# Kernel tuning notes

Measured on AMD Instinct MI355X. Metric: run time of the kernel, lower is better.

## Reference

```python
import jax, jax.numpy as jnp
import numpy as np

B, S, D, H = 2, 2048, 1024, 16
DK = D // H  # 64


def rotate_half(x):
    d = x.shape[-1]
    x1, x2 = x[..., : d // 2], x[..., d // 2 :]
    return jnp.concatenate([-x2, x1], axis=-1)


def apply_rope(q, k):
    # q, k: [B, H, S, DK]
    d_k = q.shape[-1]
    seq_len = q.shape[-2]
    theta = 10000.0 ** (-2.0 / d_k * jnp.arange(d_k // 2, dtype=q.dtype))
    positions = jnp.arange(seq_len, dtype=q.dtype)
    angles = jnp.outer(positions, theta)                    # [S, DK/2]
    cos = jnp.tile(jnp.cos(angles), (1, 2))                 # [S, DK]
    sin = jnp.tile(jnp.sin(angles), (1, 2))
    q = q * cos + rotate_half(q) * sin
    k = k * cos + rotate_half(k) * sin
    return q, k


def setup_inputs() -> dict:
    key = jax.random.key(0)
    ks = jax.random.split(key, 9)
    std = 1.0 / np.sqrt(D)
    x = jax.random.normal(ks[0], (B, S, D), dtype=jnp.float32)
    # mask True = masked (code uses masked_fill(mask, -inf)); causal mask
    mask = jnp.triu(jnp.ones((S, S), dtype=bool), k=1)[None, None, :, :]
    mask = jnp.broadcast_to(mask, (B, 1, S, S))
    Wq = jax.random.uniform(ks[1], (D, D), jnp.float32, -std, std)
    bq = jax.random.uniform(ks[2], (D,), jnp.float32, -std, std)
    Wk = jax.random.uniform(ks[3], (D, D), jnp.float32, -std, std)
    bk = jax.random.uniform(ks[4], (D,), jnp.float32, -std, std)
    Wv = jax.random.uniform(ks[5], (D, D), jnp.float32, -std, std)
    bv = jax.random.uniform(ks[6], (D,), jnp.float32, -std, std)
    Wo = jax.random.uniform(ks[7], (D, D), jnp.float32, -std, std)
    bo = jax.random.uniform(ks[8], (D,), jnp.float32, -std, std)
    return {"x": x, "mask": mask, "Wq": Wq, "bq": bq, "Wk": Wk, "bk": bk,
            "Wv": Wv, "bv": bv, "Wo": Wo, "bo": bo}


def reference(x, mask, Wq, bq, Wk, bk, Wv, bv, Wo, bo):
    b, s, d = x.shape
    # projections -> [B, H, S, DK]
    q = (x @ Wq + bq).reshape(b, s, H, DK).transpose(0, 2, 1, 3)
    k = (x @ Wk + bk).reshape(b, s, H, DK).transpose(0, 2, 1, 3)
    v = (x @ Wv + bv).reshape(b, s, H, DK).transpose(0, 2, 1, 3)
    q, k = apply_rope(q, k)
    scores = jnp.einsum("bhqd,bhkd->bhqk", q, k) / np.sqrt(DK)
    scores = jnp.where(mask, -jnp.inf, scores)
    probs = jax.nn.softmax(scores, axis=-1)
    attn = jnp.einsum("bhqk,bhkd->bhqd", probs, v)
    o = attn.transpose(0, 2, 1, 3).reshape(b, s, H * DK)
    return o @ Wo + bo
```

## Files before the change

### kernel.cpp

```cpp
#include <hip/hip_runtime.h>
#include <hip/hip_bf16.h>
#include <math.h>

typedef __hip_bfloat16 bf16;
typedef __attribute__((ext_vector_type(8))) short short8;
typedef __attribute__((ext_vector_type(4))) short s16x4;
typedef __attribute__((ext_vector_type(4))) float f32x4;

#define B_  2
#define S_  2048
#define D_  1024
#define H_  16
#define DK_ 64

#define QSCALE 0.18033688011112043f
#define EXPOFF 11.541560327111707f

__device__ inline short bfs(float f) { return __builtin_bit_cast(short, __float2bfloat16(f)); }

#define GLL16(gptr, lptr)                                                        \
    __builtin_amdgcn_global_load_lds(                                            \
        (const __attribute__((address_space(1))) void*)(gptr),                   \
        (__attribute__((address_space(3))) void*)(lptr), 16, 0, 0)

#if __has_builtin(__builtin_amdgcn_mfma_f32_16x16x16bf16_1k)
#define MFMA_16x16x16(A, Bv, C) __builtin_amdgcn_mfma_f32_16x16x16bf16_1k(A, Bv, C, 0, 0, 0)
#elif __has_builtin(__builtin_amdgcn_mfma_f32_16x16x16_bf16)
#define MFMA_16x16x16(A, Bv, C) __builtin_amdgcn_mfma_f32_16x16x16_bf16(A, Bv, C, 0, 0, 0)
#else
static __device__ inline f32x4 mfma16_asm(s16x4 a, s16x4 b, f32x4 c) {
    f32x4 d;
    asm volatile("v_mfma_f32_16x16x16_bf16 %0, %1, %2, %3\n\ts_nop 7\n\ts_nop 7"
                 : "=v"(d) : "v"(a), "v"(b), "v"(c));
    return d;
}
#define MFMA_16x16x16(A, Bv, C) mfma16_asm(A, Bv, C)
#endif

__global__ __launch_bounds__(256)
void prep_k(const float* __restrict__ x,
            const float* __restrict__ W0, const float* __restrict__ W1,
            const float* __restrict__ W2, const float* __restrict__ W3,
            bf16* __restrict__ cx, bf16* __restrict__ Wt)
{
    const int z = blockIdx.z;
    const int t = threadIdx.x;
    if (z == 4) {
        const int bid = blockIdx.y * 16 + blockIdx.x;
        #pragma unroll
        for (int i = 0; i < 16; i++) {
            const size_t g = ((size_t)bid * 256 + t) * 4 + (size_t)i * 262144;
            const float4 v = *(const float4*)(x + g);
            s16x4 o = { bfs(v.x), bfs(v.y), bfs(v.z), bfs(v.w) };
            *(s16x4*)(cx + g) = o;
        }
        return;
    }
    __shared__ float Lt[64][65];
    const float* W = (z == 0) ? W0 : (z == 1) ? W1 : (z == 2) ? W2 : W3;
    bf16* dst = Wt + (size_t)z * D_ * D_;
    const int k0 = blockIdx.y * 64, n0 = blockIdx.x * 64;
    #pragma unroll
    for (int p = 0; p < 4; p++) {
        const int idx = p * 256 + t;
        const int row = idx >> 4, cb = (idx & 15) * 4;
        const float4 v = *(const float4*)(W + (size_t)(k0 + row) * D_ + n0 + cb);
        Lt[cb + 0][row] = v.x; Lt[cb + 1][row] = v.y;
        Lt[cb + 2][row] = v.z; Lt[cb + 3][row] = v.w;
    }
    __syncthreads();
    #pragma unroll
    for (int p = 0; p < 4; p++) {
        const int idx = p * 256 + t;
        const int n = idx >> 4, kb = (idx & 15) * 4;
        s16x4 o = { bfs(Lt[n][kb]), bfs(Lt[n][kb + 1]), bfs(Lt[n][kb + 2]), bfs(Lt[n][kb + 3]) };
        *(s16x4*)(dst + (size_t)(n0 + n) * D_ + k0 + kb) = o;
    }
}

template<int MODE, int TM>
__global__ __launch_bounds__(256)
void gemm_k(const bf16* __restrict__ A, const bf16* __restrict__ WtAll,
            const float* __restrict__ b0, const float* __restrict__ b1,
            const float* __restrict__ b2,
            bf16* __restrict__ d0, bf16* __restrict__ d1, bf16* __restrict__ d2,
            float* __restrict__ fout)
{
    constexpr int K = D_;
    constexpr int MT = (B_ * S_) / TM;
    constexpr int AI = TM / 64;
    const int L = (int)blockIdx.x;
    const int m0 = (L & (MT - 1)) * TM;
    const int rest = L / MT;
    const int z = (MODE == 0) ? (rest >> 4) : 3;
    const int n0 = (MODE == 0) ? (rest & 15) * 64 : rest * 64;
    const bf16* W = WtAll + (size_t)z * D_ * D_;
    const float* bias = (MODE == 1) ? b0 : ((z == 0) ? b0 : (z == 1) ? b1 : b2);

    __shared__ __align__(16) short As[TM * 32];
    __shared__ __align__(16) short Bs[64 * 32];

    const int t = threadIdx.x;
    const int wave = t >> 6, lane = t & 63, quad = lane >> 4, l16 = lane & 15;
    const int wm = wave * (TM / 4);

    const bf16* gA0 = A + (size_t)(m0 + (t >> 2)) * K + (t & 3) * 8;
    const bf16* gA1 = gA0 + (size_t)64 * K;
    const bf16* gW0 = W + (size_t)(n0 + (t >> 2)) * K + (t & 3) * 8;
    const int wb = wave * 512;

    f32x4 acc[AI][4] = {};

    for (int k0 = 0; k0 < K; k0 += 32) {
        __syncthreads();
        GLL16(gA0 + k0, &As[wb]);
        if (TM == 128) GLL16(gA1 + k0, &As[2048 + wb]);
        GLL16(gW0 + k0, &Bs[wb]);
        __syncthreads();
        short8 af[AI], bfv[4];
        #pragma unroll
        for (int i = 0; i < AI; i++) af[i] = *(const short8*)&As[(wm + i * 16 + l16) * 32 + quad * 8];
        #pragma unroll
        for (int j = 0; j < 4; j++) bfv[j] = *(const short8*)&Bs[(j * 16 + l16) * 32 + quad * 8];
        #pragma unroll
        for (int i = 0; i < AI; i++)
            #pragma unroll
            for (int j = 0; j < 4; j++)
                acc[i][j] = __builtin_amdgcn_mfma_f32_16x16x32_bf16(af[i], bfv[j], acc[i][j], 0, 0, 0);
    }

    if (MODE == 1) {
        #pragma unroll
        for (int j = 0; j < 4; j++) {
            const int ncol = n0 + j * 16 + l16;
            const float bb = bias[ncol];
            #pragma unroll
            for (int i = 0; i < AI; i++) {
                const int mbase = m0 + wm + i * 16 + quad * 4;
                #pragma unroll
                for (int r = 0; r < 4; r++)
                    fout[(size_t)(mbase + r) * D_ + ncol] = acc[i][j][r] + bb;
            }
        }
    } else if (z == 2) {
        const int h = n0 >> 6;
        #pragma unroll
        for (int j = 0; j < 4; j++) {
            const int ncol = n0 + j * 16 + l16;
            const float bb = bias[ncol];
            const int dk = ncol & 63;
            #pragma unroll
            for (int i = 0; i < AI; i++) {
                const int mbase = m0 + wm + i * 16 + quad * 4;
                #pragma unroll
                for (int r = 0; r < 4; r++) {
                    const int m = mbase + r;
                    const int b = m >> 11, s = m & (S_ - 1);
                    d2[(((size_t)(b * H_ + h)) * DK_ + dk) * S_ + s] = __float2bfloat16(acc[i][j][r] + bb);
                }
            }
        }
    } else {
        bf16* dst = z ? d1 : d0;
        const float sc = z ? 1.0f : QSCALE;
        const int h = n0 >> 6;
        #pragma unroll
        for (int j = 0; j < 2; j++) {
            const int dk = j * 16 + l16;
            const float th = exp2f((float)dk * -0.41524101186092029f);
            const float blo = bias[(h << 6) + dk];
            const float bhi = bias[(h << 6) + dk + 32];
            #pragma unroll
            for (int i = 0; i < AI; i++) {
                #pragma unroll
                for (int r = 0; r < 4; r++) {
                    const int m = m0 + wm + i * 16 + quad * 4 + r;
                    const int b = m >> 11, s = m & (S_ - 1);
                    float sn, cs;
                    sincosf((float)s * th, &sn, &cs);
                    const float v1 = acc[i][j][r] + blo;
                    const float v2 = acc[i][j + 2][r] + bhi;
                    bf16* p = dst + (((size_t)(b * H_ + h)) * S_ + s) * DK_;
                    p[dk]      = __float2bfloat16((v1 * cs - v2 * sn) * sc);
                    p[dk + 32] = __float2bfloat16((v2 * cs + v1 * sn) * sc);
                }
            }
        }
    }
}

template<bool DIAG>
__device__ __forceinline__
void attn_tile(const short* __restrict__ Ks, const short* __restrict__ Vts,
               const short8 qf0, const short8 qf1,
               f32x4* ot, float& l_acc,
               const int wave, const int quad, const int l16)
{
    const int kkmax = DIAG ? wave : 3;
    #pragma unroll
    for (int kk = 0; kk <= kkmax; kk++) {
        const short8 kf0 = *(const short8*)&Ks[(kk * 16 + l16) * 72 + quad * 8];
        const short8 kf1 = *(const short8*)&Ks[(kk * 16 + l16) * 72 + 32 + quad * 8];
        f32x4 st = {};
        st = __builtin_amdgcn_mfma_f32_16x16x32_bf16(kf0, qf0, st, 0, 0, 0);
        st = __builtin_amdgcn_mfma_f32_16x16x32_bf16(kf1, qf1, st, 0, 0, 0);

        s16x4 pt;
        float psum = 0.0f;
        #pragma unroll
        for (int r = 0; r < 4; r++) {
            float p;
            if (DIAG) {
                const bool masked = (kk == wave) && (quad * 4 + r > l16);
                p = masked ? 0.0f : exp2f(st[r] - EXPOFF);
            } else {
                p = exp2f(st[r] - EXPOFF);
            }
            psum += p;
            pt[r] = bfs(p);
        }
        l_acc += psum;

        #pragma unroll
        for (int dt = 0; dt < 4; dt++) {
            const s16x4 vf = *(const s16x4*)&Vts[(dt * 16 + l16) * 72 + kk * 16 + quad * 4];
            ot[dt] = MFMA_16x16x16(vf, pt, ot[dt]);
        }
    }
}

__global__ __launch_bounds__(256)
void attn_k(const bf16* __restrict__ q_ws, const bf16* __restrict__ k_ws,
            const bf16* __restrict__ vt_ws, bf16* __restrict__ attn_ws)
{
    __shared__ __align__(16) short Ks[64 * 72];
    __shared__ __align__(16) short Vts[64 * 72];

    const int bh = (int)blockIdx.x;
    const int by = (int)blockIdx.y;
    const int j8 = by & 7, g = by >> 3;
    const int qt = (g == 0) ? (31 - j8) : (g == 1) ? j8 : (g == 2) ? (23 - j8) : (8 + j8);

    const int t = threadIdx.x;
    const int wave = t >> 6, quad = (t & 63) >> 4, l16 = t & 15;
    const bf16* Kb = k_ws + (size_t)bh * S_ * DK_;
    const bf16* Vb = vt_ws + (size_t)bh * DK_ * S_;
    const int b = bh >> 4, h = bh & 15;

    const bf16* Qb = q_ws + ((size_t)bh * S_ + qt * 64 + wave * 16) * DK_;
    const short8 qf0 = *(const short8*)(Qb + (size_t)l16 * DK_ + quad * 8);
    const short8 qf1 = *(const short8*)(Qb + (size_t)l16 * DK_ + 32 + quad * 8);

    float l_acc = 0.0f;
    f32x4 ot[4] = {};

    for (int kt = 0; kt <= qt; kt++) {
        __syncthreads();
        #pragma unroll
        for (int p = 0; p < 2; p++) {
            const int idx = p * 256 + t;
            const int row = idx >> 3, cb = (idx & 7) * 8;
            *(float4*)&Ks[row * 72 + cb]  = *(const float4*)(Kb + (size_t)(kt * 64 + row) * DK_ + cb);
            *(float4*)&Vts[row * 72 + cb] = *(const float4*)(Vb + (size_t)row * S_ + kt * 64 + cb);
        }
        __syncthreads();

        if (kt == qt) attn_tile<true >(Ks, Vts, qf0, qf1, ot, l_acc, wave, quad, l16);
        else          attn_tile<false>(Ks, Vts, qf0, qf1, ot, l_acc, wave, quad, l16);
    }

    l_acc += __shfl_xor(l_acc, 16, 64);
    l_acc += __shfl_xor(l_acc, 32, 64);
    const float inv = 1.0f / l_acc;
    const int srow = qt * 64 + wave * 16 + l16;
    bf16* orow = attn_ws + ((size_t)(b * S_ + srow)) * D_ + h * 64;
    #pragma unroll
    for (int dt = 0; dt < 4; dt++) {
        s16x4 o4 = { bfs(ot[dt][0] * inv), bfs(ot[dt][1] * inv),
                     bfs(ot[dt][2] * inv), bfs(ot[dt][3] * inv) };
        *(s16x4*)(orow + dt * 16 + quad * 4) = o4;
    }
}

extern "C" void kernel_launch(void* const* d_in, const int* in_sizes, int n_in,
                              void* d_out, int out_size, void* d_ws, size_t ws_size,
                              hipStream_t stream)
{
    (void)out_size; (void)ws_size;
    const float* x = nullptr;
    const float* W[4] = {nullptr, nullptr, nullptr, nullptr};
    const float* bias[4] = {nullptr, nullptr, nullptr, nullptr};
    int wi = 0, bi = 0;
    for (int i = 0; i < n_in; i++) {
        const int sz = in_sizes[i];
        if (sz == B_ * S_ * D_ && x == nullptr) x = (const float*)d_in[i];
        else if (sz == D_ * D_ && wi < 4) W[wi++] = (const float*)d_in[i];
        else if (sz == D_ && bi < 4) bias[bi++] = (const float*)d_in[i];
    }

    bf16* ws = (bf16*)d_ws;
    const size_t SEG = (size_t)B_ * S_ * D_;
    bf16* canonX  = ws;
    bf16* Wt      = ws + SEG;
    bf16* k_ws    = ws + 2 * SEG;
    bf16* vt_ws   = ws + 3 * SEG;
    bf16* attn_ws = canonX;
    bf16* q_ws    = (bf16*)d_out;

    prep_k<<<dim3(16, 16, 5), 256, 0, stream>>>(x, W[0], W[1], W[2], W[3], canonX, Wt);

    gemm_k<0, 128><<<dim3(1536, 1, 1), 256, 0, stream>>>(
        canonX, Wt, bias[0], bias[1], bias[2], q_ws, k_ws, vt_ws, nullptr);

    attn_k<<<dim3(32, 32), 256, 0, stream>>>(q_ws, k_ws, vt_ws, attn_ws);

    gemm_k<1, 64><<<dim3(1024, 1, 1), 256, 0, stream>>>(
        attn_ws, Wt, bias[3], nullptr, nullptr, nullptr, nullptr, nullptr,
        (float*)d_out);
}
```

Measured before the change: 217.5 us.

## Double-buffer K/V tiles in attention kernel with register prefetch

The attention kernel now keeps two LDS buffers for the K and V^T tiles. Global loads for the next tile are issued into registers before the current tile's compute, then written to the alternate buffer afterwards, so each iteration needs one barrier instead of two. This aims to hide global load latency behind the MFMA and softmax work. The cost is doubled LDS use and extra live registers, which may reduce occupancy.

```diff
diff --git a/kernel.cpp b/kernel.cpp
--- a/kernel.cpp
+++ b/kernel.cpp
@@ -233,8 +233,8 @@
 void attn_k(const bf16* __restrict__ q_ws, const bf16* __restrict__ k_ws,
             const bf16* __restrict__ vt_ws, bf16* __restrict__ attn_ws)
 {
-    __shared__ __align__(16) short Ks[64 * 72];
-    __shared__ __align__(16) short Vts[64 * 72];
+    __shared__ __align__(16) short Ks[2][64 * 72];
+    __shared__ __align__(16) short Vts[2][64 * 72];
 
     const int bh = (int)blockIdx.x;
     const int by = (int)blockIdx.y;
@@ -251,35 +251,57 @@
     const short8 qf0 = *(const short8*)(Qb + (size_t)l16 * DK_ + quad * 8);
     const short8 qf1 = *(const short8*)(Qb + (size_t)l16 * DK_ + 32 + quad * 8);
 
+    const int srow = t >> 3;
+    const int scb  = (t & 7) * 8;
+
+    float4 kr0, kr1, vr0, vr1;
+
+    #define STAGE_ISSUE(kt)                                                          \
+        do {                                                                         \
+            kr0 = *(const float4*)(Kb + ((size_t)(kt) * 64 + srow) * DK_ + scb);     \
+            kr1 = *(const float4*)(Kb + ((size_t)(kt) * 64 + srow + 32) * DK_ + scb);\
+            vr0 = *(const float4*)(Vb + (size_t)srow * S_ + (kt) * 64 + scb);        \
+            vr1 = *(const float4*)(Vb + (size_t)(srow + 32) * S_ + (kt) * 64 + scb); \
+        } while (0)
+
+    #define STAGE_STORE(bufi)                                                        \
+        do {                                                                         \
+            *(float4*)&Ks[bufi][srow * 72 + scb]        = kr0;                       \
+            *(float4*)&Ks[bufi][(srow + 32) * 72 + scb] = kr1;                       \
+            *(float4*)&Vts[bufi][srow * 72 + scb]       = vr0;                       \
+            *(float4*)&Vts[bufi][(srow + 32) * 72 + scb] = vr1;                      \
+        } while (0)
+
     float l_acc = 0.0f;
     f32x4 ot[4] = {};
 
+    STAGE_ISSUE(0);
+    STAGE_STORE(0);
+
     for (int kt = 0; kt <= qt; kt++) {
+        const int cur = kt & 1;
         __syncthreads();
-        #pragma unroll
-        for (int p = 0; p < 2; p++) {
-            const int idx = p * 256 + t;
-            const int row = idx >> 3, cb = (idx & 7) * 8;
-            *(float4*)&Ks[row * 72 + cb]  = *(const float4*)(Kb + (size_t)(kt * 64 + row) * DK_ + cb);
-            *(float4*)&Vts[row * 72 + cb] = *(const float4*)(Vb + (size_t)row * S_ + kt * 64 + cb);
-        }
-        __syncthreads();
-
-        if (kt == qt) attn_tile<true >(Ks, Vts, qf0, qf1, ot, l_acc, wave, quad, l16);
-        else          attn_tile<false>(Ks, Vts, qf0, qf1, ot, l_acc, wave, quad, l16);
+        if (kt < qt) STAGE_ISSUE(kt + 1);
+
+        if (kt == qt) attn_tile<true >(Ks[cur], Vts[cur], qf0, qf1, ot, l_acc, wave, quad, l16);
+        else          attn_tile<false>(Ks[cur], Vts[cur], qf0, qf1, ot, l_acc, wave, quad, l16);
+
+        if (kt < qt) STAGE_STORE(cur ^ 1);
     }
 
     l_acc += __shfl_xor(l_acc, 16, 64);
     l_acc += __shfl_xor(l_acc, 32, 64);
     const float inv = 1.0f / l_acc;
-    const int srow = qt * 64 + wave * 16 + l16;
-    bf16* orow = attn_ws + ((size_t)(b * S_ + srow)) * D_ + h * 64;
+    const int orow_s = qt * 64 + wave * 16 + l16;
+    bf16* orow = attn_ws + ((size_t)(b * S_ + orow_s)) * D_ + h * 64;
     #pragma unroll
     for (int dt = 0; dt < 4; dt++) {
         s16x4 o4 = { bfs(ot[dt][0] * inv), bfs(ot[dt][1] * inv),
                      bfs(ot[dt][2] * inv), bfs(ot[dt][3] * inv) };
         *(s16x4*)(orow + dt * 16 + quad * 4) = o4;
     }
+    #undef STAGE_ISSUE
+    #undef STAGE_STORE
 }
 
 extern "C" void kernel_launch(void* const* d_in, const int* in_sizes, int n_in,
```

Result: no change. 219.2 us (+0.8%).
